# Kernel tuning notes

Measured on AMD Instinct MI355X. Metric: run time of the kernel, lower is better.

## Reference

```python
import jax, jax.numpy as jnp
import numpy as np

N = 16384      # total nodes (16 graphs x 1024 nodes)
PG = 1024      # nodes per graph
NB = 16        # graphs in batch
E = 131072     # edges (intra-graph)
FIN = 16       # input_dim; xy coords in cols 0,1
HID = 128      # hidden_dim
H = 4          # num_heads
DH = HID // H  # per-head dim
NLAYERS = 3
NCLS = 1
NEG_SLOPE = 0.2

# D2 views: identity, flip-x, flip-y, flip-both (signs applied to xy cols 0,1)
_signs = np.ones((4, FIN), np.float32)
_signs[1, 0] = -1.0
_signs[2, 1] = -1.0
_signs[3, 0] = -1.0
_signs[3, 1] = -1.0
VIEW_SIGNS = jnp.asarray(_signs)


def setup_inputs() -> dict:
    key = jax.random.key(0)
    ks = jax.random.split(key, 16)
    x = jax.random.normal(ks[0], (N, FIN), jnp.float32)
    # intra-graph edges: dst forced into same graph block as src (matches the
    # torch per-graph edge filtering, which drops all cross-graph edges)
    src = jax.random.randint(ks[1], (E,), 0, N, dtype=jnp.int32)
    off = jax.random.randint(ks[2], (E,), 0, PG, dtype=jnp.int32)
    dst = (src // PG) * PG + off
    edge_index = jnp.stack([src, dst], axis=0)
    batch = (jnp.arange(N, dtype=jnp.int32) // PG)

    def w(k, fi, fo):
        return (jax.random.normal(k, (fi, fo), jnp.float32) / np.sqrt(fi))

    return dict(
        x=x, edge_index=edge_index, batch=batch,
        W0l=w(ks[3], FIN, HID), W0r=w(ks[4], FIN, HID),
        a0=jax.random.normal(ks[5], (H, DH), jnp.float32) / np.sqrt(DH),
        Wres0=w(ks[6], FIN, HID),
        Wl=jax.random.normal(ks[7], (NLAYERS - 1, HID, HID), jnp.float32) / np.sqrt(HID),
        Wr=jax.random.normal(ks[8], (NLAYERS - 1, HID, HID), jnp.float32) / np.sqrt(HID),
        att=jax.random.normal(ks[9], (NLAYERS - 1, H, DH), jnp.float32) / np.sqrt(DH),
        Wh1=w(ks[10], HID, HID), bh1=jnp.zeros((HID,), jnp.float32),
        Wh2=w(ks[11], HID, NCLS), bh2=jnp.zeros((NCLS,), jnp.float32),
    )


def _gatv2_layer(h, Wlk, Wrk, a, src, dst, Wres=None, act=True):
    # GATv2: e_ij = a^T LeakyReLU(Wl h_j + Wr h_i), softmax over incoming edges of i
    hl = (h @ Wlk).reshape(-1, H, DH)   # [N,H,D] source messages
    hr = (h @ Wrk).reshape(-1, H, DH)   # [N,H,D] target queries
    s = hl[src] + hr[dst]               # [E,H,D]
    e = jnp.einsum('ehd,hd->eh', jax.nn.leaky_relu(s, NEG_SLOPE), a)  # [E,H]
    m = jax.ops.segment_max(e, dst, num_segments=N)
    ex = jnp.exp(e - m[dst])
    denom = jax.ops.segment_sum(ex, dst, num_segments=N)
    alpha = ex / (denom[dst] + 1e-16)   # [E,H] per-dst softmax
    out = jax.ops.segment_sum(alpha[..., None] * hl[src], dst, num_segments=N)
    out = out.reshape(-1, H * DH)
    res = h @ Wres if Wres is not None else h
    out = out + res
    return jax.nn.elu(out) if act else out


def _backbone(xv, src, dst, W0l, W0r, a0, Wres0, Wl, Wr, att):
    h = _gatv2_layer(xv, W0l, W0r, a0, src, dst, Wres=Wres0, act=True)
    for i in range(NLAYERS - 1):
        last = (i == NLAYERS - 2)
        h = _gatv2_layer(h, Wl[i], Wr[i], att[i], src, dst, Wres=None, act=not last)
    return h


def reference(x, edge_index, batch, W0l, W0r, a0, Wres0, Wl, Wr, att, Wh1, bh1, Wh2, bh2):
    src, dst = edge_index[0], edge_index[1]
    # 4 D2 views of node features (sign flips on xy columns); vmap over views
    x4 = x[None, :, :] * VIEW_SIGNS[:, None, :]  # [4,N,FIN]
    emb4 = jax.vmap(lambda xv: _backbone(xv, src, dst, W0l, W0r, a0, Wres0, Wl, Wr, att))(x4)  # [4,N,HID]
    node_emb = emb4.mean(axis=0)  # mean over D2 views -> [N,HID]
    logits = jax.nn.relu(node_emb @ Wh1 + bh1) @ Wh2 + bh2  # [N,NCLS]
    return logits
```

## Files before the change

### kernel.cpp

```cpp
#include <hip/hip_runtime.h>
#include <hip/hip_bf16.h>
#include <math.h>

#define NN 16384
#define EE 131072
#define FIN 16
#define HID 128
#define NEG_SLOPE 0.2f

__global__ void count_kernel(const int* __restrict__ dst, int* __restrict__ deg) {
    int e = blockIdx.x * 256 + threadIdx.x;
    atomicAdd(&deg[dst[e]], 1);
}

__global__ __launch_bounds__(1024) void scan_kernel(int* __restrict__ degw ,
                                                    int* __restrict__ ptr) {
    __shared__ int sums[1024];
    int t = threadIdx.x;
    int base = t * 16;
    int local[16];
    int s = 0;
#pragma unroll
    for (int i = 0; i < 16; i++) { local[i] = degw[base + i]; s += local[i]; }
    sums[t] = s;
    __syncthreads();
    for (int off = 1; off < 1024; off <<= 1) {
        int v = (t >= off) ? sums[t - off] : 0;
        __syncthreads();
        sums[t] += v;
        __syncthreads();
    }
    int ex = (t == 0) ? 0 : sums[t - 1];
#pragma unroll
    for (int i = 0; i < 16; i++) {
        ptr[base + i] = ex;
        degw[base + i] = ex;
        ex += local[i];
    }
    if (t == 1023) ptr[NN] = sums[1023];
}

__global__ void scatter_kernel(const int* __restrict__ src, const int* __restrict__ dst,
                               int* __restrict__ ptrw, int* __restrict__ csr_src) {
    int e = blockIdx.x * 256 + threadIdx.x;
    int p = atomicAdd(&ptrw[dst[e]], 1);
    csr_src[p] = src[e];
}

#define L0_BLOCKS 2048
__global__ __launch_bounds__(256) void l0_kernel(const float* __restrict__ x,
                                                 const float* __restrict__ W0l,
                                                 const float* __restrict__ W0r,
                                                 const float* __restrict__ Wres,
                                                 float* __restrict__ hl,
                                                 float* __restrict__ hr,
                                                 float* __restrict__ hres,
                                                 int viewBase, long totalRows) {
    int tid = threadIdx.x;
    int c2 = (tid & 63) * 2;
    float2 wl2[FIN], wr2[FIN], ws2[FIN];
#pragma unroll
    for (int k = 0; k < FIN; k++) {
        wl2[k] = *(const float2*)(W0l + k * HID + c2);
        wr2[k] = *(const float2*)(W0r + k * HID + c2);
        ws2[k] = *(const float2*)(Wres + k * HID + c2);
    }
    for (long lw = (long)blockIdx.x * 4 + (tid >> 6); lw < totalRows;
         lw += (long)L0_BLOCKS * 4) {
        int v = viewBase + (int)(lw >> 14);
        int n = (int)(lw & (NN - 1));
        const float* xr = x + (long)n * FIN;
        float al0 = 0.f, al1 = 0.f, ar0 = 0.f, ar1 = 0.f, as0 = 0.f, as1 = 0.f;
#pragma unroll
        for (int k = 0; k < FIN; k++) {
            float xk = xr[k];
            if (k == 0 && (v & 1)) xk = -xk;
            if (k == 1 && (v & 2)) xk = -xk;
            al0 += xk * wl2[k].x; al1 += xk * wl2[k].y;
            ar0 += xk * wr2[k].x; ar1 += xk * wr2[k].y;
            as0 += xk * ws2[k].x; as1 += xk * ws2[k].y;
        }
        long base = lw * HID + c2;
        *(float2*)(hl + base)   = make_float2(al0, al1);
        *(float2*)(hr + base)   = make_float2(ar0, ar1);
        *(float2*)(hres + base) = make_float2(as0, as1);
    }
}

__global__ __launch_bounds__(256) void attn_kernel(const float* __restrict__ hl,
                                                   const float* __restrict__ hr,
                                                   const float* __restrict__ res,
                                                   const int* __restrict__ ptr,
                                                   const int* __restrict__ csr_src,
                                                   const float* __restrict__ avec,
                                                   float* __restrict__ hout,
                                                   int act,
                                                   int gvPerXcd) {
    int xcd = blockIdx.x & 7;
    int slot = blockIdx.x >> 3;
    int gv = xcd * gvPerXcd + (slot >> 8);
    int within = slot & 255;
    int gw = (gv << 10) + (within << 2) + (threadIdx.x >> 6);
    int l = threadIdx.x & 63;
    int n = gw & (NN - 1);
    int col = ((l >> 4) << 5) + ((l & 15) << 1);
    long base = (long)gw * HID;
    float2 hr2 = *(const float2*)(hr + base + col);
    float2 a2 = *(const float2*)(avec + col);
    float m = -INFINITY, ssum = 0.f, acc0 = 0.f, acc1 = 0.f;
    int beg = ptr[n], end = ptr[n + 1];
    long vbase = (long)(gw >> 14) * NN * HID;
    int j = beg;
    for (; j + 1 < end; j += 2) {
        int sa = csr_src[j];
        int sb = csr_src[j + 1];
        float2 ha = *(const float2*)(hl + vbase + (long)sa * HID + col);
        float2 hb = *(const float2*)(hl + vbase + (long)sb * HID + col);
        float sa0 = ha.x + hr2.x, sa1 = ha.y + hr2.y;
        float sb0 = hb.x + hr2.x, sb1 = hb.y + hr2.y;
        float ta0 = sa0 > 0.f ? sa0 : NEG_SLOPE * sa0;
        float ta1 = sa1 > 0.f ? sa1 : NEG_SLOPE * sa1;
        float tb0 = sb0 > 0.f ? sb0 : NEG_SLOPE * sb0;
        float tb1 = sb1 > 0.f ? sb1 : NEG_SLOPE * sb1;
        float p1 = ta0 * a2.x + ta1 * a2.y;
        float p2 = tb0 * a2.x + tb1 * a2.y;
        p1 += __shfl_xor(p1, 1, 16);
        p2 += __shfl_xor(p2, 1, 16);
        p1 += __shfl_xor(p1, 2, 16);
        p2 += __shfl_xor(p2, 2, 16);
        p1 += __shfl_xor(p1, 4, 16);
        p2 += __shfl_xor(p2, 4, 16);
        p1 += __shfl_xor(p1, 8, 16);
        p2 += __shfl_xor(p2, 8, 16);
        float m12 = fmaxf(p1, p2);
        float w1 = __expf(p1 - m12);
        float w2 = __expf(p2 - m12);
        float mn = fmaxf(m, m12);
        float cold = __expf(m - mn);
        float c12 = __expf(m12 - mn);
        ssum = ssum * cold + (w1 + w2) * c12;
        acc0 = acc0 * cold + (w1 * ha.x + w2 * hb.x) * c12;
        acc1 = acc1 * cold + (w1 * ha.y + w2 * hb.y) * c12;
        m = mn;
    }
    if (j < end) {
        int sa = csr_src[j];
        float2 ha = *(const float2*)(hl + vbase + (long)sa * HID + col);
        float s0 = ha.x + hr2.x, s1 = ha.y + hr2.y;
        float t0 = s0 > 0.f ? s0 : NEG_SLOPE * s0;
        float t1 = s1 > 0.f ? s1 : NEG_SLOPE * s1;
        float p = t0 * a2.x + t1 * a2.y;
        p += __shfl_xor(p, 1, 16);
        p += __shfl_xor(p, 2, 16);
        p += __shfl_xor(p, 4, 16);
        p += __shfl_xor(p, 8, 16);
        float mn = fmaxf(m, p);
        float cold = __expf(m - mn);
        float wnew = __expf(p - mn);
        ssum = ssum * cold + wnew;
        acc0 = acc0 * cold + wnew * ha.x;
        acc1 = acc1 * cold + wnew * ha.y;
        m = mn;
    }
    float inv = 1.f / (ssum + 1e-16f);
    float2 r2 = *(const float2*)(res + base + col);
    float o0 = acc0 * inv + r2.x;
    float o1 = acc1 * inv + r2.y;
    if (act) {
        o0 = o0 > 0.f ? o0 : expm1f(o0);
        o1 = o1 > 0.f ? o1 : expm1f(o1);
    }
    *(float2*)(hout + base + col) = make_float2(o0, o1);
}

#define KC 32
__global__ __launch_bounds__(256) void gemm128(const float* __restrict__ A,
                                               const float* __restrict__ B0,
                                               const float* __restrict__ B1,
                                               float* __restrict__ C0,
                                               float* __restrict__ C1,
                                               const float* __restrict__ bias,
                                               int doRelu) {
    const float* B = (blockIdx.z == 0) ? B0 : B1;
    float* C = (blockIdx.z == 0) ? C0 : C1;
    __shared__ float As[128][36];
    __shared__ float Bs[KC][132];
    int tid = threadIdx.x;
    int tx = tid & 15;
    int ty = tid >> 4;
    long row0 = (long)blockIdx.x * 128;
    float acc[8][8];
#pragma unroll
    for (int r = 0; r < 8; r++)
#pragma unroll
        for (int j = 0; j < 8; j++) acc[r][j] = 0.f;

    for (int kc = 0; kc < HID; kc += KC) {
#pragma unroll
        for (int i = 0; i < 4; i++) {
            int idx = tid + i * 256;
            int r = idx >> 3;
            int k4 = (idx & 7) * 4;
            float4 vv = *(const float4*)(A + (row0 + r) * HID + kc + k4);
            *(float4*)(&As[r][k4]) = vv;
        }
#pragma unroll
        for (int i = 0; i < 4; i++) {
            int idx = tid + i * 256;
            int kk = idx >> 5;
            int c4 = (idx & 31) * 4;
            float4 vv = *(const float4*)(B + (kc + kk) * HID + c4);
            *(float4*)(&Bs[kk][c4]) = vv;
        }
        __syncthreads();
#pragma unroll
        for (int k4 = 0; k4 < KC; k4 += 4) {
            float4 a[8];
            float4 b[4][2];
#pragma unroll
            for (int r = 0; r < 8; r++) a[r] = *(const float4*)(&As[ty + 16 * r][k4]);
#pragma unroll
            for (int kk = 0; kk < 4; kk++) {
                b[kk][0] = *(const float4*)(&Bs[k4 + kk][tx * 4]);
                b[kk][1] = *(const float4*)(&Bs[k4 + kk][64 + tx * 4]);
            }
#pragma unroll
            for (int kk = 0; kk < 4; kk++) {
#pragma unroll
                for (int r = 0; r < 8; r++) {
                    float av = reinterpret_cast<const float*>(&a[r])[kk];
                    acc[r][0] += av * b[kk][0].x;
                    acc[r][1] += av * b[kk][0].y;
                    acc[r][2] += av * b[kk][0].z;
                    acc[r][3] += av * b[kk][0].w;
                    acc[r][4] += av * b[kk][1].x;
                    acc[r][5] += av * b[kk][1].y;
                    acc[r][6] += av * b[kk][1].z;
                    acc[r][7] += av * b[kk][1].w;
                }
            }
        }
        __syncthreads();
    }
#pragma unroll
    for (int r = 0; r < 8; r++) {
        long row = row0 + ty + 16 * r;
        float o[8];
#pragma unroll
        for (int j = 0; j < 4; j++) {
            float val = acc[r][j];
            if (bias) val += bias[tx * 4 + j];
            if (doRelu) val = fmaxf(val, 0.f);
            o[j] = val;
        }
#pragma unroll
        for (int j = 4; j < 8; j++) {
            float val = acc[r][j];
            if (bias) val += bias[64 + tx * 4 + (j - 4)];
            if (doRelu) val = fmaxf(val, 0.f);
            o[j] = val;
        }
        float* crow = C + row * HID + tx * 4;
        *(float4*)crow = make_float4(o[0], o[1], o[2], o[3]);
        *(float4*)(crow + 64) = make_float4(o[4], o[5], o[6], o[7]);
    }
}

__global__ void acc_kernel(const float* __restrict__ h, float* __restrict__ emb, int k) {
    int i = blockIdx.x * 256 + threadIdx.x;
    const float4* h4 = (const float4*)h;
    float4 s = make_float4(0.f, 0.f, 0.f, 0.f);
    for (int lv = 0; lv < k; lv++) {
        float4 a = h4[i + (long)lv * NN * 32];
        s.x += a.x; s.y += a.y; s.z += a.z; s.w += a.w;
    }
    float4* e4 = (float4*)emb;
    float4 o = e4[i];
    o.x += 0.25f * s.x; o.y += 0.25f * s.y; o.z += 0.25f * s.z; o.w += 0.25f * s.w;
    e4[i] = o;
}

__global__ void logits_kernel(const float* __restrict__ z, const float* __restrict__ Wh2,
                              const float* __restrict__ bh2, float* __restrict__ out) {
    int w = (blockIdx.x * 256 + threadIdx.x) >> 6;
    int l = threadIdx.x & 63;
    float v = z[(long)w * HID + l] * Wh2[l] + z[(long)w * HID + 64 + l] * Wh2[64 + l];
    v += __shfl_xor(v, 32);
    v += __shfl_xor(v, 16);
    v += __shfl_xor(v, 8);
    v += __shfl_xor(v, 4);
    v += __shfl_xor(v, 2);
    v += __shfl_xor(v, 1);
    if (l == 0) out[w] = v + bh2[0];
}

extern "C" void kernel_launch(void* const* d_in, const int* in_sizes, int n_in,
                              void* d_out, int out_size, void* d_ws, size_t ws_size,
                              hipStream_t stream) {
    const float* x    = (const float*)d_in[0];
    const int*   ei   = (const int*)d_in[1];
    const float* W0l  = (const float*)d_in[3];
    const float* W0r  = (const float*)d_in[4];
    const float* a0   = (const float*)d_in[5];
    const float* Wres0= (const float*)d_in[6];
    const float* Wl   = (const float*)d_in[7];
    const float* Wr   = (const float*)d_in[8];
    const float* att  = (const float*)d_in[9];
    const float* Wh1  = (const float*)d_in[10];
    const float* bh1  = (const float*)d_in[11];
    const float* Wh2  = (const float*)d_in[12];
    const float* bh2  = (const float*)d_in[13];
    float* out = (float*)d_out;

    const int* src = ei;
    const int* dst = ei + EE;

    char* wsb = (char*)d_ws;
    float* emb = (float*)wsb;
    size_t off = (size_t)NN * HID * 4;
    int* ptr  = (int*)(wsb + off);  off += (NN + 1) * 4;
    int* ptrw = (int*)(wsb + off);  off += NN * 4;
    int* csr  = (int*)(wsb + off);  off += (size_t)EE * 4;
    off = (off + 255) & ~(size_t)255;
    size_t fixedBytes = off;

    int k = 4;
    while (k > 1 && fixedBytes + 3ull * k * NN * HID * 4 > ws_size) k >>= 1;
    long K = (long)k * NN;
    int npass = 4 / k;
    int gvPerXcd = (int)(K / 1024) / 8;

    float* bufA = (float*)(wsb + off);
    float* bufB = bufA + K * HID;
    float* bufC = bufB + K * HID;

    hipMemsetAsync(ptrw, 0, NN * sizeof(int), stream);
    count_kernel<<<EE / 256, 256, 0, stream>>>(dst, ptrw);
    scan_kernel<<<1, 1024, 0, stream>>>(ptrw, ptr);
    scatter_kernel<<<EE / 256, 256, 0, stream>>>(src, dst, ptrw, csr);

    hipMemsetAsync(emb, 0, (size_t)NN * HID * sizeof(float), stream);

    for (int p = 0; p < npass; p++) {
        int viewBase = p * k;
        l0_kernel<<<L0_BLOCKS, 256, 0, stream>>>(x, W0l, W0r, Wres0, bufA, bufB, bufC,
                                                 viewBase, K);
        attn_kernel<<<K / 4, 256, 0, stream>>>(bufA, bufB, bufC, ptr, csr, a0, bufB, 1, gvPerXcd);
        gemm128<<<dim3(K / 128, 1, 2), 256, 0, stream>>>(bufB, Wl, Wr, bufA, bufC, nullptr, 0);
        attn_kernel<<<K / 4, 256, 0, stream>>>(bufA, bufC, bufB, ptr, csr, att, bufC, 1, gvPerXcd);
        gemm128<<<dim3(K / 128, 1, 2), 256, 0, stream>>>(bufC, Wl + HID * HID, Wr + HID * HID,
                                                         bufA, bufB, nullptr, 0);
        attn_kernel<<<K / 4, 256, 0, stream>>>(bufA, bufB, bufC, ptr, csr, att + HID, bufB, 0, gvPerXcd);
        acc_kernel<<<NN * 32 / 256, 256, 0, stream>>>(bufB, emb, k);
    }

    gemm128<<<dim3(NN / 128, 1, 1), 256, 0, stream>>>(emb, Wh1, Wh1, bufA, bufA, bh1, 1);
    logits_kernel<<<NN * 64 / 256, 256, 0, stream>>>(bufA, Wh2, bh2, out);
}
```

Before: 438.4 us.

## Replace fp32 SIMT GEMM with split-bf16 MFMA GEMM using pre-split weights

The 128x128 dense GEMMs now run on MFMA 16x16x32 bf16 instructions instead of scalar fp32 FMA loops. Each fp32 value is split into bf16 hi and lo parts, and three MFMA products (hi*hi, hi*lo, lo*hi) approximate fp32 accuracy. Weights are pre-split once by a new kernel into a fragment-ordered layout. A operands are loaded straight from global memory without LDS staging, which risks uncoalesced loads and slightly lower precision than true fp32.

```diff
diff --git a/kernel.cpp b/kernel.cpp
--- a/kernel.cpp
+++ b/kernel.cpp
@@ -7,6 +7,14 @@
 #define FIN 16
 #define HID 128
 #define NEG_SLOPE 0.2f
+
+typedef float  floatx4 __attribute__((ext_vector_type(4)));
+typedef short  shortx8 __attribute__((ext_vector_type(8)));
+
+__device__ inline unsigned bf_hi_bits(float x) {
+    unsigned u = __float_as_uint(x);
+    return (u + 0x7FFFu + ((u >> 16) & 1u)) >> 16;
+}
 
 __global__ void count_kernel(const int* __restrict__ dst, int* __restrict__ deg) {
     int e = blockIdx.x * 256 + threadIdx.x;
@@ -45,6 +53,29 @@
     int e = blockIdx.x * 256 + threadIdx.x;
     int p = atomicAdd(&ptrw[dst[e]], 1);
     csr_src[p] = src[e];
+}
+
+__global__ void wsplit_kernel(const float* __restrict__ Wl, const float* __restrict__ Wr,
+                              const float* __restrict__ Wh1,
+                              unsigned short* __restrict__ hi, unsigned short* __restrict__ lo) {
+    int mat = blockIdx.y;
+    const float* W = (mat == 0) ? Wl : (mat == 1) ? Wr : (mat == 2) ? Wl + HID * HID
+                   : (mat == 3) ? Wr + HID * HID : Wh1;
+    int ct = blockIdx.x;
+    int t = threadIdx.x;
+    int kt = t >> 6, l = t & 63;
+    long obase = (((long)mat * 32 + (ct * 4 + kt)) * 64 + l) * 8;
+    int c = ct * 16 + (l & 15);
+    int kbase = kt * 32 + ((l >> 4) << 3);
+#pragma unroll
+    for (int j = 0; j < 8; j++) {
+        float x = W[(kbase + j) * HID + c];
+        unsigned hb = bf_hi_bits(x);
+        float r = x - __uint_as_float(hb << 16);
+        unsigned lb = bf_hi_bits(r);
+        hi[obase + j] = (unsigned short)hb;
+        lo[obase + j] = (unsigned short)lb;
+    }
 }
 
 #define L0_BLOCKS 2048
@@ -173,96 +204,78 @@
     *(float2*)(hout + base + col) = make_float2(o0, o1);
 }
 
-#define KC 32
-__global__ __launch_bounds__(256) void gemm128(const float* __restrict__ A,
-                                               const float* __restrict__ B0,
-                                               const float* __restrict__ B1,
-                                               float* __restrict__ C0,
-                                               float* __restrict__ C1,
-                                               const float* __restrict__ bias,
-                                               int doRelu) {
-    const float* B = (blockIdx.z == 0) ? B0 : B1;
+__global__ __launch_bounds__(256) void gemm_mfma(const float* __restrict__ A,
+                                                 const unsigned short* __restrict__ whi,
+                                                 const unsigned short* __restrict__ wlo,
+                                                 int mat0, int mat1,
+                                                 float* __restrict__ C0, float* __restrict__ C1,
+                                                 const float* __restrict__ bias, int doRelu) {
+    int mat = (blockIdx.z == 0) ? mat0 : mat1;
     float* C = (blockIdx.z == 0) ? C0 : C1;
-    __shared__ float As[128][36];
-    __shared__ float Bs[KC][132];
+    const unsigned short* bh = whi + (long)mat * 16384;
+    const unsigned short* bl = wlo + (long)mat * 16384;
     int tid = threadIdx.x;
-    int tx = tid & 15;
-    int ty = tid >> 4;
-    long row0 = (long)blockIdx.x * 128;
-    float acc[8][8];
-#pragma unroll
-    for (int r = 0; r < 8; r++)
-#pragma unroll
-        for (int j = 0; j < 8; j++) acc[r][j] = 0.f;
-
-    for (int kc = 0; kc < HID; kc += KC) {
-#pragma unroll
-        for (int i = 0; i < 4; i++) {
-            int idx = tid + i * 256;
-            int r = idx >> 3;
-            int k4 = (idx & 7) * 4;
-            float4 vv = *(const float4*)(A + (row0 + r) * HID + kc + k4);
-            *(float4*)(&As[r][k4]) = vv;
+    int w = tid >> 6, l = tid & 63;
+    int rh = w >> 1, ch = w & 1;
+    long row0 = (long)blockIdx.x * 128 + rh * 64;
+    int lr = l & 15;
+    int lk = (l >> 4) << 3;
+    floatx4 acc[4][4];
+#pragma unroll
+    for (int i = 0; i < 4; i++)
+#pragma unroll
+        for (int j = 0; j < 4; j++) acc[i][j] = (floatx4)0.f;
+
+    for (int kt = 0; kt < 4; kt++) {
+        shortx8 bhf[4], blf[4];
+#pragma unroll
+        for (int ctl = 0; ctl < 4; ctl++) {
+            int ct = ch * 4 + ctl;
+            long fi = ((long)(ct * 4 + kt) * 64 + l) * 8;
+            bhf[ctl] = *(const shortx8*)(bh + fi);
+            blf[ctl] = *(const shortx8*)(bl + fi);
         }
 #pragma unroll
-        for (int i = 0; i < 4; i++) {
-            int idx = tid + i * 256;
-            int kk = idx >> 5;
-            int c4 = (idx & 31) * 4;
-            float4 vv = *(const float4*)(B + (kc + kk) * HID + c4);
-            *(float4*)(&Bs[kk][c4]) = vv;
+        for (int rt = 0; rt < 4; rt++) {
+            const float* ap = A + (row0 + rt * 16 + lr) * HID + kt * 32 + lk;
+            float4 x0 = *(const float4*)(ap);
+            float4 x1 = *(const float4*)(ap + 4);
+            float xs[8] = {x0.x, x0.y, x0.z, x0.w, x1.x, x1.y, x1.z, x1.w};
+            shortx8 ah, al;
+#pragma unroll
+            for (int i = 0; i < 8; i++) {
+                unsigned hb = bf_hi_bits(xs[i]);
+                float r = xs[i] - __uint_as_float(hb << 16);
+                unsigned lb = bf_hi_bits(r);
+                ah[i] = (short)hb;
+                al[i] = (short)lb;
+            }
+#pragma unroll
+            for (int ctl = 0; ctl < 4; ctl++)
+                acc[rt][ctl] = __builtin_amdgcn_mfma_f32_16x16x32_bf16(ah, bhf[ctl], acc[rt][ctl], 0, 0, 0);
+#pragma unroll
+            for (int ctl = 0; ctl < 4; ctl++)
+                acc[rt][ctl] = __builtin_amdgcn_mfma_f32_16x16x32_bf16(ah, blf[ctl], acc[rt][ctl], 0, 0, 0);
+#pragma unroll
+            for (int ctl = 0; ctl < 4; ctl++)
+                acc[rt][ctl] = __builtin_amdgcn_mfma_f32_16x16x32_bf16(al, bhf[ctl], acc[rt][ctl], 0, 0, 0);
         }
-        __syncthreads();
-#pragma unroll
-        for (int k4 = 0; k4 < KC; k4 += 4) {
-            float4 a[8];
-            float4 b[4][2];
-#pragma unroll
-            for (int r = 0; r < 8; r++) a[r] = *(const float4*)(&As[ty + 16 * r][k4]);
-#pragma unroll
-            for (int kk = 0; kk < 4; kk++) {
-                b[kk][0] = *(const float4*)(&Bs[k4 + kk][tx * 4]);
-                b[kk][1] = *(const float4*)(&Bs[k4 + kk][64 + tx * 4]);
-            }
-#pragma unroll
-            for (int kk = 0; kk < 4; kk++) {
-#pragma unroll
-                for (int r = 0; r < 8; r++) {
-                    float av = reinterpret_cast<const float*>(&a[r])[kk];
-                    acc[r][0] += av * b[kk][0].x;
-                    acc[r][1] += av * b[kk][0].y;
-                    acc[r][2] += av * b[kk][0].z;
-                    acc[r][3] += av * b[kk][0].w;
-                    acc[r][4] += av * b[kk][1].x;
-                    acc[r][5] += av * b[kk][1].y;
-                    acc[r][6] += av * b[kk][1].z;
-                    acc[r][7] += av * b[kk][1].w;
-                }
+    }
+    int lrow4 = (l >> 4) * 4;
+#pragma unroll
+    for (int rt = 0; rt < 4; rt++) {
+#pragma unroll
+        for (int ctl = 0; ctl < 4; ctl++) {
+            int col = ch * 64 + ctl * 16 + lr;
+            float badd = bias ? bias[col] : 0.f;
+#pragma unroll
+            for (int rg = 0; rg < 4; rg++) {
+                long row = row0 + rt * 16 + lrow4 + rg;
+                float v = acc[rt][ctl][rg] + badd;
+                if (doRelu) v = fmaxf(v, 0.f);
+                C[row * HID + col] = v;
             }
         }
-        __syncthreads();
-    }
-#pragma unroll
-    for (int r = 0; r < 8; r++) {
-        long row = row0 + ty + 16 * r;
-        float o[8];
-#pragma unroll
-        for (int j = 0; j < 4; j++) {
-            float val = acc[r][j];
-            if (bias) val += bias[tx * 4 + j];
-            if (doRelu) val = fmaxf(val, 0.f);
-            o[j] = val;
-        }
-#pragma unroll
-        for (int j = 4; j < 8; j++) {
-            float val = acc[r][j];
-            if (bias) val += bias[64 + tx * 4 + (j - 4)];
-            if (doRelu) val = fmaxf(val, 0.f);
-            o[j] = val;
-        }
-        float* crow = C + row * HID + tx * 4;
-        *(float4*)crow = make_float4(o[0], o[1], o[2], o[3]);
-        *(float4*)(crow + 64) = make_float4(o[4], o[5], o[6], o[7]);
     }
 }
 
@@ -322,6 +335,9 @@
     int* ptrw = (int*)(wsb + off);  off += NN * 4;
     int* csr  = (int*)(wsb + off);  off += (size_t)EE * 4;
     off = (off + 255) & ~(size_t)255;
+    unsigned short* whi = (unsigned short*)(wsb + off); off += 5 * 16384 * 2;
+    unsigned short* wlo = (unsigned short*)(wsb + off); off += 5 * 16384 * 2;
+    off = (off + 255) & ~(size_t)255;
     size_t fixedBytes = off;
 
     int k = 4;
@@ -338,6 +354,7 @@
     count_kernel<<<EE / 256, 256, 0, stream>>>(dst, ptrw);
     scan_kernel<<<1, 1024, 0, stream>>>(ptrw, ptr);
     scatter_kernel<<<EE / 256, 256, 0, stream>>>(src, dst, ptrw, csr);
+    wsplit_kernel<<<dim3(8, 5), 256, 0, stream>>>(Wl, Wr, Wh1, whi, wlo);
 
     hipMemsetAsync(emb, 0, (size_t)NN * HID * sizeof(float), stream);
 
@@ -346,14 +363,16 @@
         l0_kernel<<<L0_BLOCKS, 256, 0, stream>>>(x, W0l, W0r, Wres0, bufA, bufB, bufC,
                                                  viewBase, K);
         attn_kernel<<<K / 4, 256, 0, stream>>>(bufA, bufB, bufC, ptr, csr, a0, bufB, 1, gvPerXcd);
-        gemm128<<<dim3(K / 128, 1, 2), 256, 0, stream>>>(bufB, Wl, Wr, bufA, bufC, nullptr, 0);
+        gemm_mfma<<<dim3(K / 128, 1, 2), 256, 0, stream>>>(bufB, whi, wlo, 0, 1,
+                                                           bufA, bufC, nullptr, 0);
         attn_kernel<<<K / 4, 256, 0, stream>>>(bufA, bufC, bufB, ptr, csr, att, bufC, 1, gvPerXcd);
-        gemm128<<<dim3(K / 128, 1, 2), 256, 0, stream>>>(bufC, Wl + HID * HID, Wr + HID * HID,
-                                                         bufA, bufB, nullptr, 0);
+        gemm_mfma<<<dim3(K / 128, 1, 2), 256, 0, stream>>>(bufC, whi, wlo, 2, 3,
+                                                           bufA, bufB, nullptr, 0);
         attn_kernel<<<K / 4, 256, 0, stream>>>(bufA, bufB, bufC, ptr, csr, att + HID, bufB, 0, gvPerXcd);
         acc_kernel<<<NN * 32 / 256, 256, 0, stream>>>(bufB, emb, k);
     }
 
-    gemm128<<<dim3(NN / 128, 1, 1), 256, 0, stream>>>(emb, Wh1, Wh1, bufA, bufA, bh1, 1);
+    gemm_mfma<<<dim3(NN / 128, 1, 1), 256, 0, stream>>>(emb, whi, wlo, 4, 4,
+                                                        bufA, bufA, bh1, 1);
     logits_kernel<<<NN * 64 / 256, 256, 0, stream>>>(bufA, Wh2, bh2, out);
 }
```

Measured after the change: 393.3 us. 10.3% less time.
